# Kernel tuning notes

Measured on AMD Instinct MI355X. Metric: run time of the kernel, lower is better.

The kernel has to match this reference:

```python
import jax, jax.numpy as jnp
import numpy as np

B, C, H, W = 1, 8192, 32, 32
C8 = C // 8  # 1024 == H*W; required by the (b,hw,hw)/(b,c8) broadcast in the original code


def setup_inputs() -> dict:
    key = jax.random.key(0)
    ks = jax.random.split(key, 11)
    rn = lambda i, shape, s=1.0: jax.random.normal(ks[i], shape, dtype=jnp.float32) * s
    return {
        "x": rn(0, (B, C, H, W)),
        "Wq": rn(1, (C8, C), 0.02),
        "Wk": rn(2, (C8, C), 0.02),
        "Wv": rn(3, (C, C), 0.02),
        "q_scale": jax.random.uniform(ks[4], (C8,), minval=0.5, maxval=1.5),
        "q_shift": rn(5, (C8,), 0.1),
        "k_scale": jax.random.uniform(ks[6], (C8,), minval=0.5, maxval=1.5),
        "k_shift": rn(7, (C8,), 0.1),
        "v_scale": jax.random.uniform(ks[8], (C,), minval=0.5, maxval=1.5),
        "v_shift": rn(9, (C,), 0.1),
        "gamma": rn(10, (), 0.5),
    }


def reference(x, Wq, Wk, Wv, q_scale, q_shift, k_scale, k_shift, v_scale, v_shift, gamma):
    b, c, h, w = x.shape
    n = h * w
    xf = x.reshape(b, c, n)  # (b, c, n)
    # BasicConv2d = 1x1 conv (no bias) + BatchNorm2d; BN folded to per-channel scale/shift
    q = jnp.einsum('oc,bcn->bon', Wq, xf) * q_scale[:, None] + q_shift[:, None]  # (b, c8, n)
    k = jnp.einsum('oc,bcn->bon', Wk, xf) * k_scale[:, None] + k_shift[:, None]  # (b, c8, n)
    v = jnp.einsum('oc,bcn->bon', Wv, xf) * v_scale[:, None] + v_shift[:, None]  # (b, c,  n)
    q = q.transpose(0, 2, 1)  # (b, n, c8)
    # PPMCC score: per-channel centering, covariance across channels
    q_c = q - q.mean(axis=1, keepdims=True)
    k_c = k - k.mean(axis=2, keepdims=True)
    cov = jnp.einsum('bnc,bcm->bnm', q_c, k_c) / (n - 1)  # (b, n, n)
    q_std = q.std(axis=1)  # (b, c8), ddof=0 (matches torch unbiased=False)
    k_std = k.std(axis=2)  # (b, c8)
    ppmcc = cov / (q_std * k_std)  # broadcasts over last axis since c8 == n
    att = jax.nn.softmax(ppmcc, axis=-1).transpose(0, 2, 1)  # (b, n, n)
    out = jnp.einsum('bcn,bnm->bcm', v, att).reshape(b, c, h, w)
    return gamma * out + x
```

## Files before the change

### kernel.cpp

```cpp
#include <hip/hip_runtime.h>
#include <cstdint>
#include <cstddef>

#define CDIM 8192
#define NDIM 1024
#define C8D  1024
#define MSTACK 10240

typedef __bf16 bf16_t;
typedef __bf16 bf16x8 __attribute__((ext_vector_type(8)));
typedef __bf16 bf16x4 __attribute__((ext_vector_type(4)));
typedef float  f32x4  __attribute__((ext_vector_type(4)));

__device__ __forceinline__ void gload_lds16(const void* g, void* l) {
    __builtin_amdgcn_global_load_lds((const __attribute__((address_space(1))) void*)g,
                                     (__attribute__((address_space(3))) void*)l, 16, 0, 0);
}

__global__ __launch_bounds__(256) void cvt_bf16_k(const float* __restrict__ in,
                                                  bf16_t* __restrict__ out, int n8) {
    int idx = blockIdx.x * 256 + threadIdx.x;
    int stride = gridDim.x * 256;
    for (int i = idx; i < n8; i += stride) {
        size_t off = (size_t)i * 8;
        float4 a = *(const float4*)(in + off);
        float4 b = *(const float4*)(in + off + 4);
        bf16x8 o = { (__bf16)a.x, (__bf16)a.y, (__bf16)a.z, (__bf16)a.w,
                     (__bf16)b.x, (__bf16)b.y, (__bf16)b.z, (__bf16)b.w };
        *(bf16x8*)(out + off) = o;
    }
}

__global__ __launch_bounds__(256) void transpose_cvt_x(const float* __restrict__ x,
                                                       bf16_t* __restrict__ xT) {
    __shared__ float t[32][33];
    const int n0 = blockIdx.x * 32, c0 = blockIdx.y * 32;
    const int tx = threadIdx.x, ty = threadIdx.y;
    #pragma unroll
    for (int i = 0; i < 4; ++i)
        t[ty + i * 8][tx] = x[(size_t)(c0 + ty + i * 8) * NDIM + n0 + tx];
    __syncthreads();
    #pragma unroll
    for (int i = 0; i < 4; ++i)
        xT[(size_t)(n0 + ty + i * 8) * CDIM + c0 + tx] = (__bf16)t[tx][ty + i * 8];
}

__global__ __launch_bounds__(256) void mega_gemm(
    const bf16_t* __restrict__ Wv, const bf16_t* __restrict__ Wq,
    const bf16_t* __restrict__ Wk, const bf16_t* __restrict__ Bx,
    bf16_t* __restrict__ v_out, float* __restrict__ q_out, float* __restrict__ k_out,
    const float* __restrict__ v_scale, const float* __restrict__ v_shift,
    const float* __restrict__ q_scale, const float* __restrict__ q_shift,
    const float* __restrict__ k_scale, const float* __restrict__ k_shift)
{
    const int lin = blockIdx.y * 8 + blockIdx.x;
    const int tile = (lin & 7) * 80 + (lin >> 3);
    const int row0 = (tile >> 3) * 128;
    const int col0 = (tile & 7) * 128;

    const bf16_t* A; const float* s0; const float* s1;
    int arow; int path;
    if (row0 < 8192)      { A = Wv; arow = row0;        s0 = v_scale; s1 = v_shift; path = 0; }
    else if (row0 < 9216) { A = Wq; arow = row0 - 8192; s0 = q_scale; s1 = q_shift; path = 1; }
    else                  { A = Wk; arow = row0 - 9216; s0 = k_scale; s1 = k_shift; path = 2; }

    const int tid = threadIdx.x;
    __shared__ __align__(16) bf16_t As[2 * 4096];
    __shared__ __align__(16) bf16_t Bs[2 * 4096];

    const int lane = tid & 63;
    const int w    = tid >> 6;
    const int wm   = (w >> 1) * 64;
    const int wn   = (w & 1) * 64;
    const int lr   = lane & 15;
    const int kg   = (lane >> 4) * 8;

    f32x4 acc[4][4];
    #pragma unroll
    for (int a_ = 0; a_ < 4; ++a_)
        #pragma unroll
        for (int b_ = 0; b_ < 4; ++b_)
            acc[a_][b_] = (f32x4){0.f, 0.f, 0.f, 0.f};

    const int eA = tid * 8;
    const int eB = (256 + tid) * 8;
    const int rA = eA >> 5, cA = eA & 31;
    const int rB = eB >> 5, cB = eB & 31;

#define MEGA_STAGE(buf, kb)                                                        \
    do {                                                                           \
        gload_lds16(A  + (size_t)(arow + rA) * CDIM + (kb) + cA, As + (buf)*4096 + eA); \
        gload_lds16(A  + (size_t)(arow + rB) * CDIM + (kb) + cB, As + (buf)*4096 + eB); \
        gload_lds16(Bx + (size_t)(col0 + rA) * CDIM + (kb) + cA, Bs + (buf)*4096 + eA); \
        gload_lds16(Bx + (size_t)(col0 + rB) * CDIM + (kb) + cB, Bs + (buf)*4096 + eB); \
    } while (0)

    MEGA_STAGE(0, 0);
    __syncthreads();
    int cur = 0;
    for (int kb = 0; kb < CDIM; kb += 32) {
        if (kb + 32 < CDIM) MEGA_STAGE(cur ^ 1, kb + 32);
        const bf16_t* Ac = As + cur * 4096;
        const bf16_t* Bc = Bs + cur * 4096;

        bf16x8 av[4], bv[4];
        #pragma unroll
        for (int mi = 0; mi < 4; ++mi)
            av[mi] = *(const bf16x8*)(Ac + (wm + mi * 16 + lr) * 32 + kg);
        #pragma unroll
        for (int ni = 0; ni < 4; ++ni)
            bv[ni] = *(const bf16x8*)(Bc + (wn + ni * 16 + lr) * 32 + kg);

        #pragma unroll
        for (int mi = 0; mi < 4; ++mi)
            #pragma unroll
            for (int ni = 0; ni < 4; ++ni)
                acc[mi][ni] = __builtin_amdgcn_mfma_f32_16x16x32_bf16(
                    av[mi], bv[ni], acc[mi][ni], 0, 0, 0);
        __syncthreads();
        cur ^= 1;
    }
#undef MEGA_STAGE

    const int cr = (lane >> 4) * 4;
    #pragma unroll
    for (int mi = 0; mi < 4; ++mi) {
        #pragma unroll
        for (int ni = 0; ni < 4; ++ni) {
            const int j = col0 + wn + ni * 16 + lr;
            #pragma unroll
            for (int r = 0; r < 4; ++r) {
                const int il = arow + wm + mi * 16 + cr + r;
                float v = acc[mi][ni][r] * s0[il] + s1[il];
                if (path == 0)      v_out[(size_t)il * NDIM + j] = (__bf16)v;
                else if (path == 1) q_out[(size_t)il * NDIM + j] = v;
                else                k_out[(size_t)il * NDIM + j] = v;
            }
        }
    }
}

template <int EPI, typename OutT>
__global__ __launch_bounds__(256) void gemm_bt(
    const bf16_t* __restrict__ A, const bf16_t* __restrict__ B,
    OutT* __restrict__ C, int M, int N, int K,
    const float* __restrict__ e0, const float* __restrict__ e1,
    const float* __restrict__ gs)
{
    const int gx = gridDim.x;
    const int nwg = gx * gridDim.y;
    const int lin = blockIdx.y * gx + blockIdx.x;
    int tile = lin;
    if ((nwg & 7) == 0) tile = (lin & 7) * (nwg >> 3) + (lin >> 3);
    const int row0 = (tile / gx) * 128;
    const int col0 = (tile % gx) * 128;

    const int Ks  = K / gridDim.z;
    const int kb0 = blockIdx.z * Ks;
    const int kb1 = kb0 + Ks;
    OutT* Cz = C + (size_t)blockIdx.z * M * N;

    const int tid = threadIdx.x;
    __shared__ __align__(16) bf16_t As[2 * 4096];
    __shared__ __align__(16) bf16_t Bs[2 * 4096];

    const int lane = tid & 63;
    const int w    = tid >> 6;
    const int wm   = (w >> 1) * 64;
    const int wn   = (w & 1) * 64;
    const int lr   = lane & 15;
    const int kg   = (lane >> 4) * 8;

    f32x4 acc[4][4];
    #pragma unroll
    for (int a_ = 0; a_ < 4; ++a_)
        #pragma unroll
        for (int b_ = 0; b_ < 4; ++b_)
            acc[a_][b_] = (f32x4){0.f, 0.f, 0.f, 0.f};

    const int eA = tid * 8;
    const int eB = (256 + tid) * 8;
    const int rA = eA >> 5, cA = eA & 31;
    const int rB = eB >> 5, cB = eB & 31;

#define BT_STAGE(buf, kb)                                                       \
    do {                                                                        \
        gload_lds16(A + (size_t)(row0 + rA) * K + (kb) + cA, As + (buf)*4096 + eA); \
        gload_lds16(A + (size_t)(row0 + rB) * K + (kb) + cB, As + (buf)*4096 + eB); \
        gload_lds16(B + (size_t)(col0 + rA) * K + (kb) + cA, Bs + (buf)*4096 + eA); \
        gload_lds16(B + (size_t)(col0 + rB) * K + (kb) + cB, Bs + (buf)*4096 + eB); \
    } while (0)

    BT_STAGE(0, kb0);
    __syncthreads();
    int cur = 0;
    for (int kb = kb0; kb < kb1; kb += 32) {
        if (kb + 32 < kb1) BT_STAGE(cur ^ 1, kb + 32);
        const bf16_t* Ac = As + cur * 4096;
        const bf16_t* Bc = Bs + cur * 4096;

        bf16x8 av[4], bv[4];
        #pragma unroll
        for (int mi = 0; mi < 4; ++mi)
            av[mi] = *(const bf16x8*)(Ac + (wm + mi * 16 + lr) * 32 + kg);
        #pragma unroll
        for (int ni = 0; ni < 4; ++ni)
            bv[ni] = *(const bf16x8*)(Bc + (wn + ni * 16 + lr) * 32 + kg);

        #pragma unroll
        for (int mi = 0; mi < 4; ++mi)
            #pragma unroll
            for (int ni = 0; ni < 4; ++ni)
                acc[mi][ni] = __builtin_amdgcn_mfma_f32_16x16x32_bf16(
                    av[mi], bv[ni], acc[mi][ni], 0, 0, 0);
        __syncthreads();
        cur ^= 1;
    }
#undef BT_STAGE

    float g = 0.f;
    if (EPI == 3) g = gs[0];
    const int cr = (lane >> 4) * 4;
    #pragma unroll
    for (int mi = 0; mi < 4; ++mi) {
        #pragma unroll
        for (int ni = 0; ni < 4; ++ni) {
            const int j = col0 + wn + ni * 16 + lr;
            float s0 = 0.f, s1 = 0.f;
            if (EPI == 2) { s0 = e0[j]; s1 = e1[j]; }
            #pragma unroll
            for (int r = 0; r < 4; ++r) {
                const int i = row0 + wm + mi * 16 + cr + r;
                float v = acc[mi][ni][r];
                if (EPI == 2)      v = v * (1.0f / 1023.0f) / (s0 * s1);
                else if (EPI == 3) v = g * v + e0[(size_t)i * N + j];
                Cz[(size_t)i * N + j] = (OutT)v;
            }
        }
    }
}

__global__ __launch_bounds__(256) void rowstats(
    const float* __restrict__ Q, const float* __restrict__ Km,
    float* __restrict__ qmean, float* __restrict__ qstd,
    float* __restrict__ kmean, float* __restrict__ kstd)
{
    const int wid  = blockIdx.x * 4 + (threadIdx.x >> 6);
    const int lane = threadIdx.x & 63;
    const float* src = (wid < 1024) ? (Q + (size_t)wid * NDIM)
                                    : (Km + (size_t)(wid - 1024) * NDIM);
    float s = 0.f, s2 = 0.f;
    #pragma unroll
    for (int p = 0; p < 4; ++p) {
        float4 v = *(const float4*)(src + p * 256 + lane * 4);
        s  += v.x + v.y + v.z + v.w;
        s2 += v.x * v.x + v.y * v.y + v.z * v.z + v.w * v.w;
    }
    #pragma unroll
    for (int o = 32; o; o >>= 1) { s += __shfl_xor(s, o); s2 += __shfl_xor(s2, o); }
    if (lane == 0) {
        float m   = s / 1024.f;
        float var = fmaxf(s2 / 1024.f - m * m, 0.f);
        if (wid < 1024) { qmean[wid] = m; qstd[wid] = sqrtf(var); }
        else            { kmean[wid - 1024] = m; kstd[wid - 1024] = sqrtf(var); }
    }
}

__global__ __launch_bounds__(256) void center_tr(
    const float* __restrict__ Q, const float* __restrict__ qmu, bf16_t* __restrict__ qc,
    const float* __restrict__ Km, const float* __restrict__ kmu, bf16_t* __restrict__ kc)
{
    __shared__ float t[32][33];
    const float* M  = blockIdx.z ? Km  : Q;
    const float* mu = blockIdx.z ? kmu : qmu;
    bf16_t* O       = blockIdx.z ? kc  : qc;
    const int o0 = blockIdx.y * 32, n0 = blockIdx.x * 32;
    const int tx = threadIdx.x, ty = threadIdx.y;
    #pragma unroll
    for (int i = 0; i < 4; ++i) {
        const int o = o0 + ty + i * 8;
        t[ty + i * 8][tx] = M[(size_t)o * NDIM + n0 + tx] - mu[o];
    }
    __syncthreads();
    #pragma unroll
    for (int i = 0; i < 4; ++i)
        O[(size_t)(n0 + ty + i * 8) * C8D + o0 + tx] = (__bf16)t[tx][ty + i * 8];
}

__global__ __launch_bounds__(256) void softmax_rows(const float* __restrict__ P,
                                                    bf16_t* __restrict__ O) {
    const int row = blockIdx.x;
    const int tid = threadIdx.x;
    const size_t PL = (size_t)NDIM * NDIM / 4;
    const size_t u  = (size_t)row * (NDIM / 4) + tid;
    const float4* B = (const float4*)P;
    float4 p0 = B[u], p1 = B[u + PL], p2 = B[u + 2 * PL], p3 = B[u + 3 * PL];
    float4 v = { p0.x + p1.x + p2.x + p3.x, p0.y + p1.y + p2.y + p3.y,
                 p0.z + p1.z + p2.z + p3.z, p0.w + p1.w + p2.w + p3.w };
    float mx = fmaxf(fmaxf(v.x, v.y), fmaxf(v.z, v.w));
    #pragma unroll
    for (int o = 32; o; o >>= 1) mx = fmaxf(mx, __shfl_xor(mx, o));
    __shared__ float red[8];
    const int w = tid >> 6, lane = tid & 63;
    if (lane == 0) red[w] = mx;
    __syncthreads();
    mx = fmaxf(fmaxf(red[0], red[1]), fmaxf(red[2], red[3]));
    float e0 = __expf(v.x - mx), e1 = __expf(v.y - mx);
    float e2 = __expf(v.z - mx), e3 = __expf(v.w - mx);
    float s = e0 + e1 + e2 + e3;
    #pragma unroll
    for (int o = 32; o; o >>= 1) s += __shfl_xor(s, o);
    if (lane == 0) red[4 + w] = s;
    __syncthreads();
    s = red[4] + red[5] + red[6] + red[7];
    const float inv = 1.0f / s;
    bf16x4 o4 = { (__bf16)(e0 * inv), (__bf16)(e1 * inv),
                  (__bf16)(e2 * inv), (__bf16)(e3 * inv) };
    ((bf16x4*)(O + (size_t)row * NDIM))[tid] = o4;
}

extern "C" void kernel_launch(void* const* d_in, const int* in_sizes, int n_in,
                              void* d_out, int out_size, void* d_ws, size_t ws_size,
                              hipStream_t stream)
{
    const float* x       = (const float*)d_in[0];
    const float* Wq      = (const float*)d_in[1];
    const float* Wk      = (const float*)d_in[2];
    const float* Wv      = (const float*)d_in[3];
    const float* q_scale = (const float*)d_in[4];
    const float* q_shift = (const float*)d_in[5];
    const float* k_scale = (const float*)d_in[6];
    const float* k_shift = (const float*)d_in[7];
    const float* v_scale = (const float*)d_in[8];
    const float* v_shift = (const float*)d_in[9];
    const float* gamma   = (const float*)d_in[10];
    float* out = (float*)d_out;

    char* w = (char*)d_ws;
    bf16_t* Wv_b = (bf16_t*)w; w += (size_t)CDIM * CDIM * 2;
    bf16_t* Wq_b = (bf16_t*)w; w += (size_t)C8D  * CDIM * 2;
    bf16_t* Wk_b = (bf16_t*)w; w += (size_t)C8D  * CDIM * 2;
    bf16_t* xT   = (bf16_t*)w; w += (size_t)NDIM * CDIM * 2;
    bf16_t* v_b  = (bf16_t*)w; w += (size_t)CDIM * NDIM * 2;
    float*  q_on = (float*) w; w += (size_t)C8D * NDIM * 4;
    float*  k_on = (float*) w; w += (size_t)C8D * NDIM * 4;
    float*  P    = (float*) w; w += (size_t)4 * NDIM * NDIM * 4;
    bf16_t* qc   = (bf16_t*)w; w += (size_t)NDIM * C8D * 2;
    bf16_t* kc   = (bf16_t*)w; w += (size_t)NDIM * C8D * 2;
    bf16_t* A0   = (bf16_t*)w; w += (size_t)NDIM * NDIM * 2;
    float*  qmean = (float*)w; w += C8D * 4;
    float*  qstd  = (float*)w; w += C8D * 4;
    float*  kmean = (float*)w; w += C8D * 4;
    float*  kstd  = (float*)w; w += C8D * 4;

    cvt_bf16_k<<<2048, 256, 0, stream>>>(Wv, Wv_b, (int)((size_t)CDIM * CDIM / 8));
    cvt_bf16_k<<<2048, 256, 0, stream>>>(Wq, Wq_b, C8D * CDIM / 8);
    cvt_bf16_k<<<2048, 256, 0, stream>>>(Wk, Wk_b, C8D * CDIM / 8);
    transpose_cvt_x<<<dim3(NDIM / 32, CDIM / 32), dim3(32, 8), 0, stream>>>(x, xT);

    mega_gemm<<<dim3(8, MSTACK / 128), 256, 0, stream>>>(
        Wv_b, Wq_b, Wk_b, xT, v_b, q_on, k_on,
        v_scale, v_shift, q_scale, q_shift, k_scale, k_shift);

    rowstats<<<512, 256, 0, stream>>>(q_on, k_on, qmean, qstd, kmean, kstd);

    center_tr<<<dim3(32, 32, 2), dim3(32, 8), 0, stream>>>(
        q_on, qmean, qc, k_on, kmean, kc);

    gemm_bt<2, float><<<dim3(NDIM / 128, NDIM / 128, 4), 256, 0, stream>>>(
        qc, kc, P, NDIM, NDIM, C8D, qstd, kstd, nullptr);

    softmax_rows<<<NDIM, 256, 0, stream>>>(P, A0);

    gemm_bt<3, float><<<dim3(NDIM / 128, CDIM / 128, 1), 256, 0, stream>>>(
        v_b, A0, out, CDIM, NDIM, NDIM, x, x, gamma);
}
```

Measured before the change: 418.8 us.

## Rewrite projection GEMM with 256x256 tiles, 8 waves, swizzled LDS, deeper K

Replaces the 128x128, 4-wave projection GEMM with a 256x256 tile kernel using 512 threads, K-step 64, and an XOR-swizzled LDS layout. It keeps two LDS buffers in flight with explicit vmcnt waits and barriers, and raises MFMA issue priority around the compute sections. The goal is more data reuse per byte loaded, fewer LDS bank conflicts, and better overlap of loads with MFMA in the dominant GEMM. The cost is 128 KB of LDS and heavy register use, which limits occupancy. Only 160 workgroups are launched, which may leave some of the 256 CUs idle.

```diff
diff --git a/kernel.cpp b/kernel.cpp
--- a/kernel.cpp
+++ b/kernel.cpp
@@ -6,6 +6,7 @@
 #define NDIM 1024
 #define C8D  1024
 #define MSTACK 10240
+#define NT8 128
 
 typedef __bf16 bf16_t;
 typedef __bf16 bf16x8 __attribute__((ext_vector_type(8)));
@@ -45,7 +46,7 @@
         xT[(size_t)(n0 + ty + i * 8) * CDIM + c0 + tx] = (__bf16)t[tx][ty + i * 8];
 }
 
-__global__ __launch_bounds__(256) void mega_gemm(
+__global__ __launch_bounds__(512, 2) void mega_gemm8(
     const bf16_t* __restrict__ Wv, const bf16_t* __restrict__ Wq,
     const bf16_t* __restrict__ Wk, const bf16_t* __restrict__ Bx,
     bf16_t* __restrict__ v_out, float* __restrict__ q_out, float* __restrict__ k_out,
@@ -53,88 +54,113 @@
     const float* __restrict__ q_scale, const float* __restrict__ q_shift,
     const float* __restrict__ k_scale, const float* __restrict__ k_shift)
 {
-    const int lin = blockIdx.y * 8 + blockIdx.x;
-    const int tile = (lin & 7) * 80 + (lin >> 3);
-    const int row0 = (tile >> 3) * 128;
-    const int col0 = (tile & 7) * 128;
-
-    const bf16_t* A; const float* s0; const float* s1;
-    int arow; int path;
-    if (row0 < 8192)      { A = Wv; arow = row0;        s0 = v_scale; s1 = v_shift; path = 0; }
-    else if (row0 < 9216) { A = Wq; arow = row0 - 8192; s0 = q_scale; s1 = q_shift; path = 1; }
-    else                  { A = Wk; arow = row0 - 9216; s0 = k_scale; s1 = k_shift; path = 2; }
-
-    const int tid = threadIdx.x;
-    __shared__ __align__(16) bf16_t As[2 * 4096];
-    __shared__ __align__(16) bf16_t Bs[2 * 4096];
-
+    __shared__ __align__(16) bf16_t Ld[65536];
+
+    const int tid  = threadIdx.x;
     const int lane = tid & 63;
-    const int w    = tid >> 6;
-    const int wm   = (w >> 1) * 64;
-    const int wn   = (w & 1) * 64;
-    const int lr   = lane & 15;
-    const int kg   = (lane >> 4) * 8;
-
-    f32x4 acc[4][4];
-    #pragma unroll
-    for (int a_ = 0; a_ < 4; ++a_)
-        #pragma unroll
-        for (int b_ = 0; b_ < 4; ++b_)
-            acc[a_][b_] = (f32x4){0.f, 0.f, 0.f, 0.f};
-
-    const int eA = tid * 8;
-    const int eB = (256 + tid) * 8;
-    const int rA = eA >> 5, cA = eA & 31;
-    const int rB = eB >> 5, cB = eB & 31;
-
-#define MEGA_STAGE(buf, kb)                                                        \
-    do {                                                                           \
-        gload_lds16(A  + (size_t)(arow + rA) * CDIM + (kb) + cA, As + (buf)*4096 + eA); \
-        gload_lds16(A  + (size_t)(arow + rB) * CDIM + (kb) + cB, As + (buf)*4096 + eB); \
-        gload_lds16(Bx + (size_t)(col0 + rA) * CDIM + (kb) + cA, Bs + (buf)*4096 + eA); \
-        gload_lds16(Bx + (size_t)(col0 + rB) * CDIM + (kb) + cB, Bs + (buf)*4096 + eB); \
-    } while (0)
-
-    MEGA_STAGE(0, 0);
-    __syncthreads();
-    int cur = 0;
-    for (int kb = 0; kb < CDIM; kb += 32) {
-        if (kb + 32 < CDIM) MEGA_STAGE(cur ^ 1, kb + 32);
-        const bf16_t* Ac = As + cur * 4096;
-        const bf16_t* Bc = Bs + cur * 4096;
-
-        bf16x8 av[4], bv[4];
-        #pragma unroll
-        for (int mi = 0; mi < 4; ++mi)
-            av[mi] = *(const bf16x8*)(Ac + (wm + mi * 16 + lr) * 32 + kg);
+    const int wid  = tid >> 6;
+    const int wr   = wid >> 2;
+    const int wc   = wid & 3;
+
+    const int lin  = blockIdx.y * 4 + blockIdx.x;
+    const int tile = (lin & 7) * 20 + (lin >> 3);
+    const int trow = tile >> 2;
+    const int col0 = (tile & 3) * 256;
+
+    const bf16_t* Ag; const float* s0; const float* s1; int arow, path;
+    if (trow < 32)      { Ag = Wv; arow = trow * 256;        s0 = v_scale; s1 = v_shift; path = 0; }
+    else if (trow < 36) { Ag = Wq; arow = trow * 256 - 8192; s0 = q_scale; s1 = q_shift; path = 1; }
+    else                { Ag = Wk; arow = trow * 256 - 9216; s0 = k_scale; s1 = k_shift; path = 2; }
+
+    const int ar0 = tid >> 3;
+    const int o0  = tid * 8;
+    const int csw = (((tid & 7) ^ ((tid >> 3) & 7)) << 3);
+
+    const int aRow = (wr * 128 + (lane & 15)) * 64;
+    const int bRow = 32768 + (wc * 64 + (lane & 15)) * 64;
+    const int ac0  = (((lane >> 4) * 8)     ) ^ ((lane & 7) << 3);
+    const int ac1  = (32 + ((lane >> 4) * 8)) ^ ((lane & 7) << 3);
+
+    f32x4 acc[8][4];
+    #pragma unroll
+    for (int mi = 0; mi < 8; ++mi)
         #pragma unroll
         for (int ni = 0; ni < 4; ++ni)
-            bv[ni] = *(const bf16x8*)(Bc + (wn + ni * 16 + lr) * 32 + kg);
-
-        #pragma unroll
-        for (int mi = 0; mi < 4; ++mi)
-            #pragma unroll
-            for (int ni = 0; ni < 4; ++ni)
-                acc[mi][ni] = __builtin_amdgcn_mfma_f32_16x16x32_bf16(
-                    av[mi], bv[ni], acc[mi][ni], 0, 0, 0);
-        __syncthreads();
-        cur ^= 1;
-    }
-#undef MEGA_STAGE
-
-    const int cr = (lane >> 4) * 4;
-    #pragma unroll
-    for (int mi = 0; mi < 4; ++mi) {
+            acc[mi][ni] = (f32x4){0.f, 0.f, 0.f, 0.f};
+
+#define STAGE8(BUF, KB) do {                                                                  \
+    gload_lds16(Ag + (size_t)(arow + ar0      ) * CDIM + (KB) + csw, Ld + (BUF)*16384 + o0          ); \
+    gload_lds16(Ag + (size_t)(arow + ar0 +  64) * CDIM + (KB) + csw, Ld + (BUF)*16384 + o0 +  4096  ); \
+    gload_lds16(Ag + (size_t)(arow + ar0 + 128) * CDIM + (KB) + csw, Ld + (BUF)*16384 + o0 +  8192  ); \
+    gload_lds16(Ag + (size_t)(arow + ar0 + 192) * CDIM + (KB) + csw, Ld + (BUF)*16384 + o0 + 12288  ); \
+    gload_lds16(Bx + (size_t)(col0 + ar0      ) * CDIM + (KB) + csw, Ld + 32768 + (BUF)*16384 + o0          ); \
+    gload_lds16(Bx + (size_t)(col0 + ar0 +  64) * CDIM + (KB) + csw, Ld + 32768 + (BUF)*16384 + o0 +  4096  ); \
+    gload_lds16(Bx + (size_t)(col0 + ar0 + 128) * CDIM + (KB) + csw, Ld + 32768 + (BUF)*16384 + o0 +  8192  ); \
+    gload_lds16(Bx + (size_t)(col0 + ar0 + 192) * CDIM + (KB) + csw, Ld + 32768 + (BUF)*16384 + o0 + 12288  ); \
+} while (0)
+
+#define HALF_MMA(BUF, AC) do {                                                                \
+    bf16x8 av[8], bv[4];                                                                      \
+    _Pragma("unroll") for (int mi = 0; mi < 8; ++mi)                                          \
+        av[mi] = *(const bf16x8*)(Ld + (BUF)*16384 + aRow + mi*1024 + (AC));                  \
+    _Pragma("unroll") for (int ni = 0; ni < 4; ++ni)                                          \
+        bv[ni] = *(const bf16x8*)(Ld + (BUF)*16384 + bRow + ni*1024 + (AC));                  \
+    __builtin_amdgcn_s_setprio(1);                                                            \
+    _Pragma("unroll") for (int mi = 0; mi < 8; ++mi)                                          \
+        _Pragma("unroll") for (int ni = 0; ni < 4; ++ni)                                      \
+            acc[mi][ni] = __builtin_amdgcn_mfma_f32_16x16x32_bf16(av[mi], bv[ni],             \
+                                                                  acc[mi][ni], 0, 0, 0);      \
+    __builtin_amdgcn_s_setprio(0);                                                            \
+} while (0)
+
+#define TILE8(BUF, T) do {                                                                    \
+    HALF_MMA(BUF, ac0);                                                                       \
+    HALF_MMA(BUF, ac1);                                                                       \
+    if ((T) != NT8 - 1) {                                                                     \
+        asm volatile("s_waitcnt lgkmcnt(0)" ::: "memory");                                    \
+        __builtin_amdgcn_sched_barrier(0);                                                    \
+        __builtin_amdgcn_s_barrier();                       \
+        __builtin_amdgcn_sched_barrier(0);                                                    \
+        if ((T) + 2 < NT8) {                                                                  \
+            STAGE8(BUF, ((T) + 2) * 64);                                                      \
+            asm volatile("s_waitcnt vmcnt(8)" ::: "memory");                                  \
+        } else {                                                                              \
+            asm volatile("s_waitcnt vmcnt(0)" ::: "memory");                                  \
+        }                                                                                     \
+        __builtin_amdgcn_sched_barrier(0);                                                    \
+        __builtin_amdgcn_s_barrier();                          \
+        __builtin_amdgcn_sched_barrier(0);                                                    \
+    }                                                                                         \
+} while (0)
+
+    STAGE8(0, 0);
+    STAGE8(1, 64);
+    asm volatile("s_waitcnt vmcnt(8)" ::: "memory");
+    __builtin_amdgcn_sched_barrier(0);
+    __builtin_amdgcn_s_barrier();
+    __builtin_amdgcn_sched_barrier(0);
+
+    for (int t = 0; t < NT8; t += 2) {
+        TILE8(0, t);
+        TILE8(1, t + 1);
+    }
+#undef TILE8
+#undef HALF_MMA
+#undef STAGE8
+
+    const int cq = (lane >> 4) * 4;
+    #pragma unroll
+    for (int mi = 0; mi < 8; ++mi) {
         #pragma unroll
         for (int ni = 0; ni < 4; ++ni) {
-            const int j = col0 + wn + ni * 16 + lr;
+            const int j = col0 + wc * 64 + ni * 16 + (lane & 15);
             #pragma unroll
             for (int r = 0; r < 4; ++r) {
-                const int il = arow + wm + mi * 16 + cr + r;
-                float v = acc[mi][ni][r] * s0[il] + s1[il];
-                if (path == 0)      v_out[(size_t)il * NDIM + j] = (__bf16)v;
-                else if (path == 1) q_out[(size_t)il * NDIM + j] = v;
-                else                k_out[(size_t)il * NDIM + j] = v;
+                const int il = arow + wr * 128 + mi * 16 + cq + r;
+                float vv = acc[mi][ni][r] * s0[il] + s1[il];
+                if (path == 0)      v_out[(size_t)il * NDIM + j] = (__bf16)vv;
+                else if (path == 1) q_out[(size_t)il * NDIM + j] = vv;
+                else                k_out[(size_t)il * NDIM + j] = vv;
             }
         }
     }
@@ -358,7 +384,7 @@
     cvt_bf16_k<<<2048, 256, 0, stream>>>(Wk, Wk_b, C8D * CDIM / 8);
     transpose_cvt_x<<<dim3(NDIM / 32, CDIM / 32), dim3(32, 8), 0, stream>>>(x, xT);
 
-    mega_gemm<<<dim3(8, MSTACK / 128), 256, 0, stream>>>(
+    mega_gemm8<<<dim3(4, MSTACK / 256), 512, 0, stream>>>(
         Wv_b, Wq_b, Wk_b, xT, v_b, q_on, k_on,
         v_scale, v_shift, q_scale, q_shift, k_scale, k_shift);
 
```

Result: no change. 416.4 us (-0.6%).
